# Optimization experiments

Measured on AMD Instinct MI355X. Metric: run time of the kernel, lower is better.

Reference implementation:

```python
import jax, jax.numpy as jnp
import numpy as np
from jax import lax

B, T, D, LSTM, N_MELS, SPK, NOISE = 256, 600, 256, 512, 80, 256, 64
MAX_R = 10
FC1 = 256
FC2 = D // 2  # 128
FILTERS, KSIZE = 32, 31


def _lin(k, out_d, in_d):
    return jax.random.normal(k, (out_d, in_d), jnp.float32) * 0.02


def setup_inputs() -> dict:
    key = jax.random.key(0)
    ks = list(jax.random.split(key, 40))
    nk = iter(ks)
    inp = {
        "encoder_seq": jax.random.normal(next(nk), (B, T, D), jnp.float32),
        "encoder_seq_proj": jax.random.normal(next(nk), (B, T, D), jnp.float32),
        "prenet_in": jax.random.normal(next(nk), (B, N_MELS), jnp.float32),
        "attn_hidden": jax.random.normal(next(nk), (B, D), jnp.float32),
        "rnn1_hidden": jax.random.normal(next(nk), (B, LSTM), jnp.float32),
        "rnn2_hidden": jax.random.normal(next(nk), (B, LSTM), jnp.float32),
        "rnn1_cell": jax.random.normal(next(nk), (B, LSTM), jnp.float32),
        "rnn2_cell": jax.random.normal(next(nk), (B, LSTM), jnp.float32),
        "context_vec": jax.random.normal(next(nk), (B, D), jnp.float32),
        "speaker_embedding": jax.random.normal(next(nk), (B, SPK), jnp.float32),
        "noise_embedding": jax.random.normal(next(nk), (B, NOISE), jnp.float32),
        "attn_cumulative": jax.random.uniform(next(nk), (B, T), jnp.float32),
        "attn_prev": jax.random.uniform(next(nk), (B, T), jnp.float32),
        "phone_len": jax.random.randint(next(nk), (B,), 1, T + 1),
        # PreNet
        "fc1_w": _lin(next(nk), FC1, N_MELS + NOISE), "fc1_b": jnp.zeros((FC1,), jnp.float32),
        "fc2_w": _lin(next(nk), FC2, FC1), "fc2_b": jnp.zeros((FC2,), jnp.float32),
        # LSA
        "conv_w": jax.random.normal(next(nk), (FILTERS, 2, KSIZE), jnp.float32) * 0.1,
        "L_w": _lin(next(nk), D, FILTERS), "L_b": jnp.zeros((D,), jnp.float32),
        "W_w": _lin(next(nk), D, D), "W_b": jnp.zeros((D,), jnp.float32),
        "v_w": _lin(next(nk), 1, D),
        # attn GRU: input = D + D//2 + SPK
        "gru_wih": _lin(next(nk), 3 * D, D + FC2 + SPK), "gru_whh": _lin(next(nk), 3 * D, D),
        "gru_bih": jnp.zeros((3 * D,), jnp.float32), "gru_bhh": jnp.zeros((3 * D,), jnp.float32),
        # rnn_input Linear: 2*D + SPK + NOISE -> LSTM
        "rnn_in_w": _lin(next(nk), LSTM, 2 * D + SPK + NOISE), "rnn_in_b": jnp.zeros((LSTM,), jnp.float32),
        # two LSTMCells
        "l1_wih": _lin(next(nk), 4 * LSTM, LSTM), "l1_whh": _lin(next(nk), 4 * LSTM, LSTM),
        "l1_bih": jnp.zeros((4 * LSTM,), jnp.float32), "l1_bhh": jnp.zeros((4 * LSTM,), jnp.float32),
        "l2_wih": _lin(next(nk), 4 * LSTM, LSTM), "l2_whh": _lin(next(nk), 4 * LSTM, LSTM),
        "l2_bih": jnp.zeros((4 * LSTM,), jnp.float32), "l2_bhh": jnp.zeros((4 * LSTM,), jnp.float32),
        # mel projection (no bias)
        "mel_w": _lin(next(nk), N_MELS * MAX_R, LSTM),
        "r": 2,
    }
    return inp


def _gru(x, h, wih, whh, bih, bhh):
    gi = x @ wih.T + bih
    gh = h @ whh.T + bhh
    i_r, i_z, i_n = jnp.split(gi, 3, axis=-1)
    h_r, h_z, h_n = jnp.split(gh, 3, axis=-1)
    r = jax.nn.sigmoid(i_r + h_r)
    z = jax.nn.sigmoid(i_z + h_z)
    n = jnp.tanh(i_n + r * h_n)
    return (1.0 - z) * n + z * h


def _lstm(x, h, c, wih, whh, bih, bhh):
    g = x @ wih.T + bih + h @ whh.T + bhh
    i, f, gg, o = jnp.split(g, 4, axis=-1)
    c_new = jax.nn.sigmoid(f) * c + jax.nn.sigmoid(i) * jnp.tanh(gg)
    h_new = jax.nn.sigmoid(o) * jnp.tanh(c_new)
    return h_new, c_new


def reference(encoder_seq, encoder_seq_proj, prenet_in, attn_hidden, rnn1_hidden,
              rnn2_hidden, rnn1_cell, rnn2_cell, context_vec, speaker_embedding,
              noise_embedding, attn_cumulative, attn_prev, phone_len,
              fc1_w, fc1_b, fc2_w, fc2_b, conv_w, L_w, L_b, W_w, W_b, v_w,
              gru_wih, gru_whh, gru_bih, gru_bhh, rnn_in_w, rnn_in_b,
              l1_wih, l1_whh, l1_bih, l1_bhh, l2_wih, l2_whh, l2_bih, l2_bhh,
              mel_w, r):
    # PreNet (eval-mode: dropout omitted for a deterministic reference)
    p = jnp.concatenate([prenet_in, noise_embedding], axis=-1)
    p = jax.nn.relu(p @ fc1_w.T + fc1_b)
    prenet_out = jax.nn.relu(p @ fc2_w.T + fc2_b)

    # attention GRU
    attn_rnn_in = jnp.concatenate([context_vec, prenet_out, speaker_embedding], axis=-1)
    attn_hidden = _gru(attn_rnn_in, attn_hidden, gru_wih, gru_whh, gru_bih, gru_bhh)

    # location-sensitive attention (t > 0 step; state passed explicitly)
    pq = (attn_hidden @ W_w.T + W_b)[:, None, :]                     # [B,1,D]
    location = jnp.stack([attn_cumulative, attn_prev], axis=1)       # [B,2,T]
    loc = lax.conv_general_dilated(location, conv_w, (1,), [((KSIZE - 1) // 2,) * 2],
                                   dimension_numbers=("NCH", "OIH", "NCH"))  # [B,F,T]
    pl = jnp.einsum("bft,df->btd", loc, L_w) + L_b                   # [B,T,D]
    u = jnp.einsum("btd,od->bt", jnp.tanh(pq + encoder_seq_proj + pl), v_w)
    mask = jnp.arange(T)[None, :] < phone_len[:, None]
    u = jnp.where(mask, u, -1e9)
    scores_bt = jax.nn.softmax(u, axis=1)                            # [B,T]
    scores = scores_bt[:, None, :]                                   # [B,1,T]

    context_vec = jnp.einsum("bt,btd->bd", scores_bt, encoder_seq)   # [B,D]

    x = jnp.concatenate([context_vec, attn_hidden, speaker_embedding, noise_embedding], axis=1)
    x = x @ rnn_in_w.T + rnn_in_b

    rnn1_hidden, rnn1_cell = _lstm(x, rnn1_hidden, rnn1_cell, l1_wih, l1_whh, l1_bih, l1_bhh)
    x = x + rnn1_hidden
    rnn2_hidden, rnn2_cell = _lstm(x, rnn2_hidden, rnn2_cell, l2_wih, l2_whh, l2_bih, l2_bhh)
    x = x + rnn2_hidden

    mels = (x @ mel_w.T).reshape(B, N_MELS, MAX_R)[:, :, :r]
    return (mels, scores, attn_hidden, rnn1_hidden, rnn2_hidden, rnn1_cell, rnn2_cell, context_vec)
```

## Files before the change

kernel.cpp:

```cpp
#include <hip/hip_runtime.h>
#include <hip/hip_bf16.h>
#include <cstdint>

#define B_ 256
#define T_ 600
#define D_ 256

typedef __attribute__((ext_vector_type(8))) short bf16x8;
typedef __attribute__((ext_vector_type(4))) float f32x4;

__device__ __forceinline__ float fast_sigmoid(float x) {
    return __fdividef(1.0f, 1.0f + __expf(-x));
}
__device__ __forceinline__ float fast_tanh(float x) {
    return 1.0f - __fdividef(2.0f, __expf(2.0f * x) + 1.0f);
}
__device__ __forceinline__ ushort f2bf(float f) {
    unsigned u = __float_as_uint(f);
    u += 0x7FFF + ((u >> 16) & 1);
    return (ushort)(u >> 16);
}

__global__ __launch_bounds__(256) void prenet_kernel(
    const float* __restrict__ pre_in, const float* __restrict__ noise,
    const float* __restrict__ w1, const float* __restrict__ b1,
    const float* __restrict__ w2, const float* __restrict__ b2,
    const float* __restrict__ ctx_in, const float* __restrict__ spk,
    const float* __restrict__ L_w, ushort* __restrict__ Lw16,
    ushort* __restrict__ Xgru16, ushort* __restrict__ Xrnn16)
{
    __shared__ float xin[144];
    __shared__ float p1[256];
    int b = blockIdx.x, t = threadIdx.x;
    if (b == 0) {
        for (int o = t; o < 8192; o += 256) {
            int dt = o >> 9;
            int ln = (o >> 3) & 63;
            int j  = o & 7;
            int in_idx = (dt * 16 + (ln & 15)) * 32 + (ln >> 4) * 8 + j;
            Lw16[o] = f2bf(L_w[in_idx]);
        }
    }
    float s = spk[b * 256 + t];
    Xgru16[b * 640 + t] = f2bf(ctx_in[b * 256 + t]);
    Xgru16[b * 640 + 384 + t] = f2bf(s);
    Xrnn16[b * 832 + 512 + t] = f2bf(s);
    if (t < 64) Xrnn16[b * 832 + 768 + t] = f2bf(noise[b * 64 + t]);
    if (t < 80) xin[t] = pre_in[b * 80 + t];
    else if (t < 144) xin[t] = noise[b * 64 + (t - 80)];
    __syncthreads();
    float acc = b1[t];
    const float4* w = (const float4*)(w1 + t * 144);
    const float4* xi = (const float4*)xin;
#pragma unroll 9
    for (int k = 0; k < 36; ++k) {
        float4 wv = w[k]; float4 xv = xi[k];
        acc += wv.x * xv.x + wv.y * xv.y + wv.z * xv.z + wv.w * xv.w;
    }
    p1[t] = fmaxf(acc, 0.f);
    __syncthreads();
    if (t < 128) {
        float a2 = b2[t];
        const float4* w2v = (const float4*)(w2 + t * 256);
        const float4* pv = (const float4*)p1;
#pragma unroll 8
        for (int k = 0; k < 64; ++k) {
            float4 wv = w2v[k]; float4 xv = pv[k];
            a2 += wv.x * xv.x + wv.y * xv.y + wv.z * xv.z + wv.w * xv.w;
        }
        Xgru16[b * 640 + 256 + t] = f2bf(fmaxf(a2, 0.f));
    }
}

__global__ __launch_bounds__(256) void convert_all(
    const float* __restrict__ w1ih, const float* __restrict__ w1hh,
    const float* __restrict__ w2ih, const float* __restrict__ w2hh,
    const float* __restrict__ gwih, const float* __restrict__ gwhh,
    const float* __restrict__ Ww, const float* __restrict__ riw,
    const float* __restrict__ ahin, const float* __restrict__ h1in,
    ushort* __restrict__ wcat1, ushort* __restrict__ wcat2,
    ushort* __restrict__ gwih16, ushort* __restrict__ gwhh16,
    ushort* __restrict__ Ww16, ushort* __restrict__ riw16,
    ushort* __restrict__ ahin16, ushort* __restrict__ xh1)
{
    int bid = blockIdx.x, t = threadIdx.x;
    if (bid < 4096) {
        int n = bid & 2047;
        int layer = bid >> 11;
        const float* wih = layer ? w2ih : w1ih;
        const float* whh = layer ? w2hh : w1hh;
        ushort* dst = layer ? wcat2 : wcat1;
        const float* src = (t < 128) ? (wih + (size_t)n * 512 + t * 4)
                                     : (whh + (size_t)n * 512 + (t - 128) * 4);
        float4 v = *(const float4*)src;
        ushort4 o;
        o.x = f2bf(v.x); o.y = f2bf(v.y); o.z = f2bf(v.z); o.w = f2bf(v.w);
        *(ushort4*)&dst[(size_t)n * 1024 + t * 4] = o;
        return;
    }
    bid -= 4096;
    if (bid >= 1216) {
        bid -= 1216;
        size_t i = (size_t)bid * 1024 + t * 4;
        float4 v = *(const float4*)&h1in[i];
        int b = (int)(i >> 9), k = (int)(i & 511);
        ushort4 o;
        o.x = f2bf(v.x); o.y = f2bf(v.y); o.z = f2bf(v.z); o.w = f2bf(v.w);
        *(ushort4*)&xh1[(size_t)b * 1024 + 512 + k] = o;
        return;
    }
    const float* src; ushort* dst;
    if (bid < 480)       { src = gwih; dst = gwih16; }
    else if (bid < 672)  { bid -= 480;  src = gwhh; dst = gwhh16; }
    else if (bid < 736)  { bid -= 672;  src = Ww;   dst = Ww16; }
    else if (bid < 1152) { bid -= 736;  src = riw;  dst = riw16; }
    else                 { bid -= 1152; src = ahin; dst = ahin16; }
    size_t i = (size_t)bid * 1024 + t * 4;
    float4 v = *(const float4*)&src[i];
    ushort4 o;
    o.x = f2bf(v.x); o.y = f2bf(v.y); o.z = f2bf(v.z); o.w = f2bf(v.w);
    *(ushort4*)&dst[i] = o;
}

__global__ __launch_bounds__(256) void mfma_gemmN(
    const ushort* __restrict__ A16, int K,
    const ushort* __restrict__ B16, const float* __restrict__ bias,
    float* __restrict__ C, int N, ushort* __restrict__ xcast)
{
    int tid = threadIdx.x;
    int lane = tid & 63, wv = tid >> 6;
    int m0 = blockIdx.x * 32;
    int n0 = blockIdx.y * 64;
    int wm = wv >> 1, wn = wv & 1;
    int cl = lane & 15, ko = (lane >> 4) * 8;

    const ushort* ap  = A16 + (size_t)(m0 + wm * 16 + cl) * K + ko;
    const ushort* bp0 = B16 + (size_t)(n0 + wn * 32 + cl) * K + ko;
    const ushort* bp1 = bp0 + (size_t)16 * K;

    f32x4 acc0 = {0.f, 0.f, 0.f, 0.f};
    f32x4 acc1 = {0.f, 0.f, 0.f, 0.f};
    int nks = K >> 5;
#pragma unroll 2
    for (int ks = 0; ks < nks; ++ks) {
        bf16x8 a  = *(const bf16x8*)ap;
        bf16x8 b0 = *(const bf16x8*)bp0;
        bf16x8 b1 = *(const bf16x8*)bp1;
        ap += 32; bp0 += 32; bp1 += 32;
        acc0 = __builtin_amdgcn_mfma_f32_16x16x32_bf16(a, b0, acc0, 0, 0, 0);
        acc1 = __builtin_amdgcn_mfma_f32_16x16x32_bf16(a, b1, acc1, 0, 0, 0);
    }
    int orow = m0 + wm * 16 + (lane >> 4) * 4;
    int ocol = n0 + wn * 32 + cl;
    float bb0 = bias ? bias[ocol] : 0.f;
    float bb1 = bias ? bias[ocol + 16] : 0.f;
#pragma unroll
    for (int r2 = 0; r2 < 4; ++r2) {
        float v0 = acc0[r2] + bb0;
        float v1 = acc1[r2] + bb1;
        C[(size_t)(orow + r2) * N + ocol]      = v0;
        C[(size_t)(orow + r2) * N + ocol + 16] = v1;
        if (xcast) {
            xcast[(size_t)(orow + r2) * 1024 + ocol]      = f2bf(v0);
            xcast[(size_t)(orow + r2) * 1024 + ocol + 16] = f2bf(v1);
        }
    }
}

__global__ __launch_bounds__(256) void mfma_gemm(
    const ushort* __restrict__ A16, const ushort* __restrict__ B16,
    float* __restrict__ G0, float* __restrict__ G1)
{
    int tid = threadIdx.x;
    int lane = tid & 63, wv = tid >> 6;
    int m0 = blockIdx.x * 32;
    int n0 = blockIdx.y * 64;
    int kbase = blockIdx.z * 512;
    float* Gout = blockIdx.z ? G1 : G0;
    int wm = wv >> 1, wn = wv & 1;
    int cl = lane & 15, ko = (lane >> 4) * 8;

    const ushort* ap  = A16 + (size_t)(m0 + wm * 16 + cl) * 1024 + kbase + ko;
    const ushort* bp0 = B16 + (size_t)(n0 + wn * 32 + cl) * 1024 + kbase + ko;
    const ushort* bp1 = bp0 + (size_t)16 * 1024;

    f32x4 acc0 = {0.f, 0.f, 0.f, 0.f};
    f32x4 acc1 = {0.f, 0.f, 0.f, 0.f};
#pragma unroll
    for (int ks = 0; ks < 16; ++ks) {
        bf16x8 a  = *(const bf16x8*)(ap  + ks * 32);
        bf16x8 b0 = *(const bf16x8*)(bp0 + ks * 32);
        bf16x8 b1 = *(const bf16x8*)(bp1 + ks * 32);
        acc0 = __builtin_amdgcn_mfma_f32_16x16x32_bf16(a, b0, acc0, 0, 0, 0);
        acc1 = __builtin_amdgcn_mfma_f32_16x16x32_bf16(a, b1, acc1, 0, 0, 0);
    }
    int orow = m0 + wm * 16 + (lane >> 4) * 4;
    int ocol = n0 + wn * 32 + cl;
#pragma unroll
    for (int r2 = 0; r2 < 4; ++r2) {
        Gout[(size_t)(orow + r2) * 2048 + ocol]      = acc0[r2];
        Gout[(size_t)(orow + r2) * 2048 + ocol + 16] = acc1[r2];
    }
}

__global__ __launch_bounds__(256) void gru_combine(
    const float* __restrict__ Cgi, const float* __restrict__ Cgh,
    const float* __restrict__ h_in, float* __restrict__ ah_out,
    ushort* __restrict__ ah16, ushort* __restrict__ Xrnn16)
{
    int b = blockIdx.x, j = threadIdx.x;
    float gir = Cgi[b * 768 + j], giz = Cgi[b * 768 + 256 + j], gin = Cgi[b * 768 + 512 + j];
    float ghr = Cgh[b * 768 + j], ghz = Cgh[b * 768 + 256 + j], ghn = Cgh[b * 768 + 512 + j];
    float rr = fast_sigmoid(gir + ghr);
    float zz = fast_sigmoid(giz + ghz);
    float nn = fast_tanh(gin + rr * ghn);
    float h = (1.f - zz) * nn + zz * h_in[b * 256 + j];
    ah_out[b * 256 + j] = h;
    ah16[b * 256 + j] = f2bf(h);
    Xrnn16[b * 832 + 256 + j] = f2bf(h);
}

__global__ __launch_bounds__(1024) void attn_u_kernel(
    const float* __restrict__ esp, const float* __restrict__ pq,
    const float* __restrict__ cum, const float* __restrict__ prv,
    const float* __restrict__ conv_w, const ushort* __restrict__ Lw16,
    const float* __restrict__ L_b, const float* __restrict__ v_w,
    float* __restrict__ u)
{
    __shared__ float cumL[96], prvL[96];
    __shared__ float cwL[1984];
    __shared__ ushort lwS[8192];
    __shared__ ushort locs[64][40];
    __shared__ float pq2s[256], vvs[256];
    __shared__ float upart[4][64];
    int b = blockIdx.y;
    int t0 = blockIdx.x * 64;
    int tid = threadIdx.x;
    int lane = tid & 63, w = tid >> 6;
    int tt = w & 3, dtg = w >> 2;
    int cl = lane & 15, gr = lane >> 4;

    int tw = t0 + tt * 16 + cl;
    int tc = (tw < T_) ? tw : (T_ - 1);
    const float4* ep4 = (const float4*)(esp + ((size_t)b * T_ + tc) * 256) + gr;
    float4 e0 = ep4[(dtg * 4 + 0) * 4];
    float4 e1 = ep4[(dtg * 4 + 1) * 4];
    float4 e2 = ep4[(dtg * 4 + 2) * 4];
    float4 e3 = ep4[(dtg * 4 + 3) * 4];

    for (int i = tid; i < 94; i += 1024) {
        int tg = t0 + i - 15;
        bool ok = (tg >= 0) && (tg < T_);
        cumL[i] = ok ? cum[b * T_ + tg] : 0.f;
        prvL[i] = ok ? prv[b * T_ + tg] : 0.f;
    }
    for (int i = tid; i < 1984; i += 1024) cwL[i] = conv_w[i];
    {
        const float4* src = (const float4*)Lw16;
        float4* dst = (float4*)lwS;
        dst[tid] = src[tid];
    }
    if (tid < 256) {
        pq2s[tid] = pq[b * 256 + tid] + L_b[tid];
        vvs[tid] = v_w[tid];
    }
    __syncthreads();

    {
        int f = tid & 31, ts = tid >> 5;
        const float* c0 = &cwL[f * 62];
        float a0 = 0.f, a1 = 0.f;
#pragma unroll
        for (int k = 0; k < 31; ++k) {
            float wcv = c0[k], wpv = c0[31 + k];
            a0 = fmaf(cumL[ts + k], wcv, fmaf(prvL[ts + k], wpv, a0));
            a1 = fmaf(cumL[ts + 32 + k], wcv, fmaf(prvL[ts + 32 + k], wpv, a1));
        }
        locs[ts][f] = f2bf(a0);
        locs[ts + 32][f] = f2bf(a1);
    }
    __syncthreads();

    bf16x8 locf = *(const bf16x8*)&locs[tt * 16 + cl][gr * 8];
    float sum = 0.f;
    int dt0 = dtg * 4;
#define STEP(J, EV)                                                           \
    {                                                                         \
        int dt = dt0 + (J);                                                   \
        bf16x8 af = *(const bf16x8*)&lwS[(dt * 64 + lane) * 8];               \
        float4 pq4 = *(const float4*)&pq2s[dt * 16 + gr * 4];                 \
        float4 vv4 = *(const float4*)&vvs[dt * 16 + gr * 4];                  \
        f32x4 acc = {pq4.x, pq4.y, pq4.z, pq4.w};                             \
        acc = __builtin_amdgcn_mfma_f32_16x16x32_bf16(af, locf, acc, 0, 0, 0);\
        sum = fmaf(fast_tanh(EV.x + acc[0]), vv4.x, sum);                     \
        sum = fmaf(fast_tanh(EV.y + acc[1]), vv4.y, sum);                     \
        sum = fmaf(fast_tanh(EV.z + acc[2]), vv4.z, sum);                     \
        sum = fmaf(fast_tanh(EV.w + acc[3]), vv4.w, sum);                     \
    }
    STEP(0, e0)
    STEP(1, e1)
    STEP(2, e2)
    STEP(3, e3)
#undef STEP
    sum += __shfl_xor(sum, 16, 64);
    sum += __shfl_xor(sum, 32, 64);
    if (lane < 16) upart[dtg][tt * 16 + cl] = sum;
    __syncthreads();
    if (tid < 64) {
        int t = t0 + tid;
        if (t < T_)
            u[b * T_ + t] = upart[0][tid] + upart[1][tid] + upart[2][tid] + upart[3][tid];
    }
}

__global__ __launch_bounds__(1024) void softmax_ctx_kernel(
    const float* __restrict__ u, const int* __restrict__ plen,
    const float* __restrict__ enc,
    float* __restrict__ scores, float* __restrict__ ctx_out,
    ushort* __restrict__ Xrnn16)
{
    __shared__ float sc[T_];
    __shared__ float red[16];
    __shared__ float part[16][256];
    int b = blockIdx.x, tid = threadIdx.x;
    int lane = tid & 63, wid = tid >> 6;
    int pl = plen[b];
    float mv = -1e30f;
    if (tid < T_) {
        float uv = u[b * T_ + tid];
        mv = (tid < pl) ? uv : -1e9f;
        sc[tid] = mv;
    }
    float m = mv;
#pragma unroll
    for (int off = 32; off > 0; off >>= 1) m = fmaxf(m, __shfl_xor(m, off, 64));
    if (lane == 0) red[wid] = m;
    __syncthreads();
    m = red[0];
#pragma unroll
    for (int i = 1; i < 16; ++i) m = fmaxf(m, red[i]);
    float ev = 0.f;
    if (tid < T_) ev = __expf(sc[tid] - m);
    float s = ev;
    __syncthreads();
#pragma unroll
    for (int off = 32; off > 0; off >>= 1) s += __shfl_xor(s, off, 64);
    if (lane == 0) red[wid] = s;
    __syncthreads();
    float tot = 0.f;
#pragma unroll
    for (int i = 0; i < 16; ++i) tot += red[i];
    float inv = __fdividef(1.0f, tot);
    if (tid < T_) {
        float scv = ev * inv;
        scores[b * T_ + tid] = scv;
        sc[tid] = scv;
    }
    __syncthreads();
    float a0 = 0.f, a1 = 0.f, a2 = 0.f, a3 = 0.f;
    const float4* ep = (const float4*)(enc + ((size_t)b * T_ + wid) * 256) + lane;
    for (int t = wid; t < T_; t += 16) {
        float sv = sc[t];
        float4 ev4 = *ep;
        a0 = fmaf(sv, ev4.x, a0);
        a1 = fmaf(sv, ev4.y, a1);
        a2 = fmaf(sv, ev4.z, a2);
        a3 = fmaf(sv, ev4.w, a3);
        ep += 16 * 64;
    }
    part[wid][lane * 4 + 0] = a0;
    part[wid][lane * 4 + 1] = a1;
    part[wid][lane * 4 + 2] = a2;
    part[wid][lane * 4 + 3] = a3;
    __syncthreads();
    if (tid < 256) {
        float c = 0.f;
#pragma unroll
        for (int q = 0; q < 16; ++q) c += part[q][tid];
        ctx_out[b * 256 + tid] = c;
        Xrnn16[b * 832 + tid] = f2bf(c);
    }
}

__global__ __launch_bounds__(512) void lstm_combine2(
    const float* __restrict__ G0, const float* __restrict__ G1,
    const float* __restrict__ bih, const float* __restrict__ bhh,
    const float* __restrict__ c_in, const float* __restrict__ x_in,
    float* __restrict__ h_out, float* __restrict__ c_out,
    float* __restrict__ x_next,
    const float* __restrict__ h_next_in, ushort* __restrict__ xh_next)
{
    int b = blockIdx.x, j = threadIdx.x;
    size_t base = (size_t)b * 2048;
    float gi = G0[base + j] + G1[base + j] + bih[j] + bhh[j];
    float gf = G0[base + 512 + j] + G1[base + 512 + j] + bih[512 + j] + bhh[512 + j];
    float gg = G0[base + 1024 + j] + G1[base + 1024 + j] + bih[1024 + j] + bhh[1024 + j];
    float go = G0[base + 1536 + j] + G1[base + 1536 + j] + bih[1536 + j] + bhh[1536 + j];
    float c = fast_sigmoid(gf) * c_in[b * 512 + j] + fast_sigmoid(gi) * fast_tanh(gg);
    float h = fast_sigmoid(go) * fast_tanh(c);
    float xn = x_in[b * 512 + j] + h;
    h_out[b * 512 + j] = h;
    c_out[b * 512 + j] = c;
    x_next[b * 512 + j] = xn;
    if (xh_next) {
        xh_next[(size_t)b * 1024 + j] = f2bf(xn);
        xh_next[(size_t)b * 1024 + 512 + j] = f2bf(h_next_in[b * 512 + j]);
    }
}

__global__ __launch_bounds__(256) void mel_kernel(
    const float* __restrict__ x2, const float* __restrict__ mel_w,
    int r, float* __restrict__ mels)
{
    __shared__ float xl[512];
    int b = blockIdx.x, tid = threadIdx.x;
    xl[tid] = x2[b * 512 + tid];
    xl[256 + tid] = x2[b * 512 + 256 + tid];
    __syncthreads();
    for (int idx = tid; idx < 80 * r; idx += 256) {
        int mrow = (idx / r) * 10 + (idx % r);
        const float4* w = (const float4*)(mel_w + (size_t)mrow * 512);
        const float4* xv = (const float4*)xl;
        float acc = 0.f;
#pragma unroll 16
        for (int k = 0; k < 128; ++k) {
            float4 a = w[k], c = xv[k];
            acc += a.x * c.x + a.y * c.y + a.z * c.z + a.w * c.w;
        }
        mels[(size_t)b * 80 * r + idx] = acc;
    }
}

extern "C" void kernel_launch(void* const* d_in, const int* in_sizes, int n_in,
                              void* d_out, int out_size, void* d_ws, size_t ws_size,
                              hipStream_t stream)
{
    const float* enc    = (const float*)d_in[0];
    const float* esp    = (const float*)d_in[1];
    const float* pre_in = (const float*)d_in[2];
    const float* ah_in  = (const float*)d_in[3];
    const float* h1_in  = (const float*)d_in[4];
    const float* h2_in  = (const float*)d_in[5];
    const float* c1_in  = (const float*)d_in[6];
    const float* c2_in  = (const float*)d_in[7];
    const float* ctx_in = (const float*)d_in[8];
    const float* spk    = (const float*)d_in[9];
    const float* noise  = (const float*)d_in[10];
    const float* cum    = (const float*)d_in[11];
    const float* prv    = (const float*)d_in[12];
    const int*   plen   = (const int*)d_in[13];
    const float* fc1_w  = (const float*)d_in[14];
    const float* fc1_b  = (const float*)d_in[15];
    const float* fc2_w  = (const float*)d_in[16];
    const float* fc2_b  = (const float*)d_in[17];
    const float* conv_w = (const float*)d_in[18];
    const float* L_w    = (const float*)d_in[19];
    const float* L_b    = (const float*)d_in[20];
    const float* W_w    = (const float*)d_in[21];
    const float* W_b    = (const float*)d_in[22];
    const float* v_w    = (const float*)d_in[23];
    const float* g_wih  = (const float*)d_in[24];
    const float* g_whh  = (const float*)d_in[25];
    const float* g_bih  = (const float*)d_in[26];
    const float* g_bhh  = (const float*)d_in[27];
    const float* ri_w   = (const float*)d_in[28];
    const float* ri_b   = (const float*)d_in[29];
    const float* l1_wih = (const float*)d_in[30];
    const float* l1_whh = (const float*)d_in[31];
    const float* l1_bih = (const float*)d_in[32];
    const float* l1_bhh = (const float*)d_in[33];
    const float* l2_wih = (const float*)d_in[34];
    const float* l2_whh = (const float*)d_in[35];
    const float* l2_bih = (const float*)d_in[36];
    const float* l2_bhh = (const float*)d_in[37];
    const float* mel_w  = (const float*)d_in[38];

    int r = (out_size - 808960) / 20480;
    if (r < 1) r = 1;
    if (r > 10) r = 10;

    float* out    = (float*)d_out;
    float* mels   = out;
    float* scores = out + (size_t)20480 * r;
    float* ah_out = scores + 153600;
    float* h1_out = ah_out + 65536;
    float* h2_out = h1_out + 131072;
    float* c1_out = h2_out + 131072;
    float* c2_out = c1_out + 131072;
    float* ctx_out = c2_out + 131072;

    float* ws   = (float*)d_ws;
    float* Cgi  = ws;
    float* Cgh  = Cgi + 196608;
    float* pq   = Cgh + 196608;
    float* uu   = pq + 65536;
    float* x0   = uu + 153600;
    float* x1   = x0 + 131072;
    float* x2   = x1 + 131072;
    float* G0   = x2 + 131072;
    float* G1   = G0 + 524288;
    ushort* Lw16   = (ushort*)(G1 + 524288);
    ushort* Xgru16 = Lw16 + 8192;
    ushort* Xrnn16 = Xgru16 + 163840;
    ushort* ah16   = Xrnn16 + 212992;
    ushort* ahin16 = ah16 + 65536;
    ushort* wcat1  = ahin16 + 65536;
    ushort* wcat2  = wcat1 + 2097152;
    ushort* gwih16 = wcat2 + 2097152;
    ushort* gwhh16 = gwih16 + 491520;
    ushort* Ww16   = gwhh16 + 196608;
    ushort* riw16  = Ww16 + 65536;
    ushort* xh1    = riw16 + 425984;
    ushort* xh2    = xh1 + 262144;

    prenet_kernel<<<256, 256, 0, stream>>>(pre_in, noise, fc1_w, fc1_b, fc2_w, fc2_b,
                                           ctx_in, spk, L_w, Lw16, Xgru16, Xrnn16);
    convert_all<<<5440, 256, 0, stream>>>(l1_wih, l1_whh, l2_wih, l2_whh,
                                          g_wih, g_whh, W_w, ri_w, ah_in, h1_in,
                                          wcat1, wcat2, gwih16, gwhh16,
                                          Ww16, riw16, ahin16, xh1);
    mfma_gemmN<<<dim3(8, 12), 256, 0, stream>>>(Xgru16, 640, gwih16, g_bih, Cgi, 768, nullptr);
    mfma_gemmN<<<dim3(8, 12), 256, 0, stream>>>(ahin16, 256, gwhh16, g_bhh, Cgh, 768, nullptr);
    gru_combine<<<256, 256, 0, stream>>>(Cgi, Cgh, ah_in, ah_out, ah16, Xrnn16);
    mfma_gemmN<<<dim3(8, 4), 256, 0, stream>>>(ah16, 256, Ww16, W_b, pq, 256, nullptr);
    attn_u_kernel<<<dim3(10, 256), 1024, 0, stream>>>(esp, pq, cum, prv, conv_w, Lw16, L_b, v_w, uu);
    softmax_ctx_kernel<<<256, 1024, 0, stream>>>(uu, plen, enc, scores, ctx_out, Xrnn16);
    mfma_gemmN<<<dim3(8, 8), 256, 0, stream>>>(Xrnn16, 832, riw16, ri_b, x0, 512, xh1);
    mfma_gemm<<<dim3(8, 32, 2), 256, 0, stream>>>(xh1, wcat1, G0, G1);
    lstm_combine2<<<256, 512, 0, stream>>>(G0, G1, l1_bih, l1_bhh, c1_in, x0,
                                           h1_out, c1_out, x1, h2_in, xh2);
    mfma_gemm<<<dim3(8, 32, 2), 256, 0, stream>>>(xh2, wcat2, G0, G1);
    lstm_combine2<<<256, 512, 0, stream>>>(G0, G1, l2_bih, l2_bhh, c2_in, x1,
                                           h2_out, c2_out, x2, nullptr, nullptr);
    mel_kernel<<<256, 256, 0, stream>>>(x2, mel_w, r, mels);
}
```

Before: 199.9 us.

## Stage location projection in LDS and read encoder_seq_proj rows coalesced

The attention-energy kernel now writes the MFMA location-projection results to a padded shared-memory tile in bf16. It then reads encoder_seq_proj one full row per wave with contiguous float4 loads, instead of the scattered per-lane row loads used before. Each wave reduces its row with a full 64-lane butterfly. This removes the cross-wave upart reduction but adds an extra barrier, about 33KB more LDS (which may reduce occupancy), bf16 rounding of the projection, and a later issue of the global loads that used to be overlapped with the conv setup.

```diff
diff --git a/kernel.cpp b/kernel.cpp
--- a/kernel.cpp
+++ b/kernel.cpp
@@ -19,6 +19,9 @@
     unsigned u = __float_as_uint(f);
     u += 0x7FFF + ((u >> 16) & 1);
     return (ushort)(u >> 16);
+}
+__device__ __forceinline__ float bf2f(ushort u) {
+    return __uint_as_float((unsigned)u << 16);
 }
 
 __global__ __launch_bounds__(256) void prenet_kernel(
@@ -220,6 +223,7 @@
     Xrnn16[b * 832 + 256 + j] = f2bf(h);
 }
 
+#define PLP 264
 __global__ __launch_bounds__(1024) void attn_u_kernel(
     const float* __restrict__ esp, const float* __restrict__ pq,
     const float* __restrict__ cum, const float* __restrict__ prv,
@@ -231,22 +235,14 @@
     __shared__ float cwL[1984];
     __shared__ ushort lwS[8192];
     __shared__ ushort locs[64][40];
+    __shared__ ushort plS[64 * PLP];
     __shared__ float pq2s[256], vvs[256];
-    __shared__ float upart[4][64];
     int b = blockIdx.y;
     int t0 = blockIdx.x * 64;
     int tid = threadIdx.x;
     int lane = tid & 63, w = tid >> 6;
     int tt = w & 3, dtg = w >> 2;
     int cl = lane & 15, gr = lane >> 4;
-
-    int tw = t0 + tt * 16 + cl;
-    int tc = (tw < T_) ? tw : (T_ - 1);
-    const float4* ep4 = (const float4*)(esp + ((size_t)b * T_ + tc) * 256) + gr;
-    float4 e0 = ep4[(dtg * 4 + 0) * 4];
-    float4 e1 = ep4[(dtg * 4 + 1) * 4];
-    float4 e2 = ep4[(dtg * 4 + 2) * 4];
-    float4 e3 = ep4[(dtg * 4 + 3) * 4];
 
     for (int i = tid; i < 94; i += 1024) {
         int tg = t0 + i - 15;
@@ -281,35 +277,39 @@
     }
     __syncthreads();
 
-    bf16x8 locf = *(const bf16x8*)&locs[tt * 16 + cl][gr * 8];
-    float sum = 0.f;
-    int dt0 = dtg * 4;
-#define STEP(J, EV)                                                           \
-    {                                                                         \
-        int dt = dt0 + (J);                                                   \
-        bf16x8 af = *(const bf16x8*)&lwS[(dt * 64 + lane) * 8];               \
-        float4 pq4 = *(const float4*)&pq2s[dt * 16 + gr * 4];                 \
-        float4 vv4 = *(const float4*)&vvs[dt * 16 + gr * 4];                  \
-        f32x4 acc = {pq4.x, pq4.y, pq4.z, pq4.w};                             \
-        acc = __builtin_amdgcn_mfma_f32_16x16x32_bf16(af, locf, acc, 0, 0, 0);\
-        sum = fmaf(fast_tanh(EV.x + acc[0]), vv4.x, sum);                     \
-        sum = fmaf(fast_tanh(EV.y + acc[1]), vv4.y, sum);                     \
-        sum = fmaf(fast_tanh(EV.z + acc[2]), vv4.z, sum);                     \
-        sum = fmaf(fast_tanh(EV.w + acc[3]), vv4.w, sum);                     \
-    }
-    STEP(0, e0)
-    STEP(1, e1)
-    STEP(2, e2)
-    STEP(3, e3)
-#undef STEP
-    sum += __shfl_xor(sum, 16, 64);
-    sum += __shfl_xor(sum, 32, 64);
-    if (lane < 16) upart[dtg][tt * 16 + cl] = sum;
-    __syncthreads();
-    if (tid < 64) {
-        int t = t0 + tid;
-        if (t < T_)
-            u[b * T_ + t] = upart[0][tid] + upart[1][tid] + upart[2][tid] + upart[3][tid];
+    {
+        bf16x8 locf = *(const bf16x8*)&locs[tt * 16 + cl][gr * 8];
+#pragma unroll
+        for (int j = 0; j < 4; ++j) {
+            int dt = dtg * 4 + j;
+            bf16x8 af = *(const bf16x8*)&lwS[(dt * 64 + lane) * 8];
+            f32x4 acc = {0.f, 0.f, 0.f, 0.f};
+            acc = __builtin_amdgcn_mfma_f32_16x16x32_bf16(af, locf, acc, 0, 0, 0);
+            ushort4 pk;
+            pk.x = f2bf(acc[0]); pk.y = f2bf(acc[1]);
+            pk.z = f2bf(acc[2]); pk.w = f2bf(acc[3]);
+            *(ushort4*)&plS[(tt * 16 + cl) * PLP + dt * 16 + gr * 4] = pk;
+        }
+    }
+    __syncthreads();
+
+    float4 pq4 = *(const float4*)&pq2s[lane * 4];
+    float4 vv4 = *(const float4*)&vvs[lane * 4];
+#pragma unroll
+    for (int rr = 0; rr < 4; ++rr) {
+        int row = w + rr * 16;
+        int tg = t0 + row;
+        int tc = (tg < T_) ? tg : (T_ - 1);
+        float4 e4 = *((const float4*)(esp + ((size_t)b * T_ + tc) * 256) + lane);
+        ushort4 pl4 = *(const ushort4*)&plS[row * PLP + lane * 4];
+        float s = 0.f;
+        s = fmaf(fast_tanh(e4.x + pq4.x + bf2f(pl4.x)), vv4.x, s);
+        s = fmaf(fast_tanh(e4.y + pq4.y + bf2f(pl4.y)), vv4.y, s);
+        s = fmaf(fast_tanh(e4.z + pq4.z + bf2f(pl4.z)), vv4.z, s);
+        s = fmaf(fast_tanh(e4.w + pq4.w + bf2f(pl4.w)), vv4.w, s);
+#pragma unroll
+        for (int off = 32; off > 0; off >>= 1) s += __shfl_xor(s, off, 64);
+        if (lane == 0 && tg < T_) u[b * T_ + tg] = s;
     }
 }
 
```

After: 207.1 us. +3.6%, slower.
